# Performance work log

Hardware: AMD Instinct MI355X
Metric: run time of the kernel (lower is better)

Reference implementation:

```python
import jax, jax.numpy as jnp
import numpy as np

B, P, H, V, E, D = 32, 24, 24, 32000, 300, 512


def setup_inputs() -> dict:
    key = jax.random.key(0)
    ks = jax.random.split(key, 16)
    f32 = jnp.float32

    def nrm(k, shape, fan):
        return jax.random.normal(k, shape, f32) / np.sqrt(fan).astype(np.float32)

    return {
        'premise': jax.random.randint(ks[0], (B, P), 0, V),
        'hypothesis': jax.random.randint(ks[1], (B, H), 0, V),
        'embedding': jax.random.normal(ks[2], (V, E), f32),
        'W_ih': nrm(ks[3], (8 * D, 2 * E), 2 * E),
        'W_hh': nrm(ks[4], (8 * D, 2 * D), 2 * D),
        'b_ih': jnp.zeros((8 * D,), f32),
        'b_hh': jnp.zeros((8 * D,), f32),
        'W_ch': nrm(ks[5], (D, 2 * D), 2 * D),
        'b_ch': jnp.zeros((D,), f32),
        'W_cc': nrm(ks[6], (D, 2 * D), 2 * D),
        'b_cc': jnp.zeros((D,), f32),
        'W1': nrm(ks[7], (D, D), D),
        'b1': jnp.zeros((D,), f32),
        'W2': nrm(ks[8], (D, D), D),
        'b2': jnp.zeros((D,), f32),
        'W3': nrm(ks[9], (3, D), D),
        'b3': jnp.zeros((3,), f32),
    }


def reference(premise, hypothesis, embedding, W_ih, W_hh, b_ih, b_hh,
              W_ch, b_ch, W_cc, b_cc, W1, b1, W2, b2, W3, b3):
    prem = embedding[premise]      # [B,P,E]
    hyp = embedding[hypothesis]    # [B,H,E]
    bsz = prem.shape[0]
    d = W_ch.shape[0]
    prem_t = prem.transpose(1, 0, 2)  # [P,B,E]
    hyp_t = hyp.transpose(1, 0, 2)    # [H,B,E]
    zero = jnp.zeros((bsz, d), prem.dtype)

    def lstm_cell(x, h, c):
        # PyTorch LSTMCell gate order: i, f, g, o
        g = x @ W_ih.T + b_ih + h @ W_hh.T + b_hh
        i, f, gg, o = jnp.split(g, 4, axis=-1)
        c2 = jax.nn.sigmoid(f) * c + jax.nn.sigmoid(i) * jnp.tanh(gg)
        h2 = jax.nn.sigmoid(o) * jnp.tanh(c2)
        return h2, c2

    def outer(row, px):
        # row holds (h,c) of the previous premise row (left neighbors), [H,B,D]
        row_h, row_c = row

        def inner(low, ins):
            lh, lc = low                 # lower neighbor (current row, j-1)
            left_h, left_c, hx = ins     # left neighbor (prev row, j) and hyp emb
            x = jnp.concatenate([px, hx], axis=-1)          # [B,2E]
            hcat = jnp.concatenate([left_h, lh], axis=-1)   # [B,2D]
            ccat = jnp.concatenate([left_c, lc], axis=-1)
            oh, oc = lstm_cell(x, hcat, ccat)
            nh = oh @ W_ch.T + b_ch      # condense to [B,D]
            nc = oc @ W_cc.T + b_cc
            return (nh, nc), (nh, nc)

        _, (nrh, nrc) = jax.lax.scan(inner, (zero, zero), (row_h, row_c, hyp_t))
        return (nrh, nrc), None

    hlen = hyp_t.shape[0]
    init = (jnp.zeros((hlen, bsz, d), prem.dtype),
            jnp.zeros((hlen, bsz, d), prem.dtype))
    (row_h, _), _ = jax.lax.scan(outer, init, prem_t)

    h = row_h[-1]                          # h at grid cell (P,H)
    h = jax.nn.relu(h @ W1.T + b1)
    h = jax.nn.relu(h @ W2.T + b2)
    return jax.nn.softmax(h @ W3.T + b3, axis=1)
```

## Files before the change

kernel.cpp:

```cpp
#include <hip/hip_runtime.h>

#define P_   24
#define H_   24
#define E_   300
#define D_   512
#define TWOD 1024
#define G4   4096
#define SMEMB  27648
#define BUFSZ  23040
#define SMEMG2 46080

typedef __attribute__((ext_vector_type(8))) short bf16x8;
typedef __attribute__((ext_vector_type(4))) float f32x4;

__device__ __forceinline__ float bf2f(unsigned int u) {
    return __uint_as_float(u << 16);
}
__device__ __forceinline__ unsigned short f2bf(float f) {
    unsigned int x = __float_as_uint(f);
    unsigned int r = (x + 0x7fffu + ((x >> 16) & 1u)) >> 16;
    return (unsigned short)r;
}
__device__ __forceinline__ float sigf(float x) {
    return 1.0f / (1.0f + __expf(-x));
}
__device__ __forceinline__ float tanh_f(float x) {
    return 2.0f / (1.0f + __expf(-2.0f * x)) - 1.0f;
}

#define OFF_WHHP 0u
#define OFF_WCHB 8388608u
#define OFF_WCCB 9437184u
#define OFF_APRE 10485760u
#define OFF_CPRE 16777216u
#define OFF_PX   23068672u
#define OFF_HX   23560192u
#define OFF_HBB  24051712u
#define OFF_CBF  25624576u
#define OFF_H2B  28770304u
#define OFF_C2B  30343168u
#define OFF_HF   31916032u
#define OFF_T1   33488896u
#define OFF_T2   33554432u

__global__ __launch_bounds__(256) void k_p0(
        const int* __restrict__ prem, const int* __restrict__ hyp,
        const float* __restrict__ emb, const float* __restrict__ Whh,
        const float* __restrict__ Wch, const float* __restrict__ Wcc,
        char* __restrict__ wsb) {
    unsigned short* WhhP = (unsigned short*)(wsb + OFF_WHHP);
    unsigned short* WchB = (unsigned short*)(wsb + OFF_WCHB);
    unsigned short* WccB = (unsigned short*)(wsb + OFF_WCCB);
    unsigned short* PX   = (unsigned short*)(wsb + OFF_PX);
    unsigned short* HX   = (unsigned short*)(wsb + OFF_HX);

    int gt = blockIdx.x * 256 + threadIdx.x;
    int stride = gridDim.x * 256;
    for (int idx = gt; idx < 524288; idx += stride) {
        int n = idx >> 7;
        int k8 = (idx & 127) * 8;
        int q = n >> 10, rest = n & 1023;
        int nt = rest >> 5, u = rest & 31;
        int pr = nt * 128 + q * 32 + u;
        const float* s = Whh + (size_t)n * TWOD + k8;
        float4 va = *(const float4*)s, vb = *(const float4*)(s + 4);
        unsigned short o[8] = {f2bf(va.x), f2bf(va.y), f2bf(va.z), f2bf(va.w),
                               f2bf(vb.x), f2bf(vb.y), f2bf(vb.z), f2bf(vb.w)};
        *(uint4*)(WhhP + (size_t)pr * TWOD + k8) = *(const uint4*)o;
    }
    for (int idx = gt; idx < 131072; idx += stride) {
        int cc = idx & 65535;
        const float* s = ((idx < 65536) ? Wch : Wcc) + (size_t)cc * 8;
        unsigned short* dp = ((idx < 65536) ? WchB : WccB) + (size_t)cc * 8;
        float4 va = *(const float4*)s, vb = *(const float4*)(s + 4);
        unsigned short o[8] = {f2bf(va.x), f2bf(va.y), f2bf(va.z), f2bf(va.w),
                               f2bf(vb.x), f2bf(vb.y), f2bf(vb.z), f2bf(vb.w)};
        *(uint4*)dp = *(const uint4*)o;
    }
    for (int idx = gt; idx < 61440; idx += stride) {
        int isH = idx >= 30720 ? 1 : 0;
        int id2 = idx - isH * 30720;
        int rb = id2 / 40, c8 = (id2 % 40) * 8;
        int ri = rb >> 5, rbb = rb & 31;
        int tok = isH ? hyp[rbb * H_ + ri] : prem[rbb * P_ + ri];
        const float* s = emb + (size_t)tok * E_ + c8;
        unsigned short o[8];
        for (int e = 0; e < 8; ++e)
            o[e] = (c8 + e < E_) ? f2bf(s[e]) : (unsigned short)0;
        *(uint4*)((isH ? HX : PX) + rb * 320 + c8) = *(const uint4*)o;
    }
}

__global__ __launch_bounds__(256) void k_p1(
        const float* __restrict__ Wih, const float* __restrict__ bih,
        const float* __restrict__ bhh, char* __restrict__ wsb) {
    const unsigned short* PX = (const unsigned short*)(wsb + OFF_PX);
    const unsigned short* HX = (const unsigned short*)(wsb + OFF_HX);
    unsigned short* Apre = (unsigned short*)(wsb + OFF_APRE);
    unsigned short* Cpre = (unsigned short*)(wsb + OFF_CPRE);

    __shared__ __align__(16) unsigned char smem[SMEMB];
    const int t = threadIdx.x;
    const int lane = t & 63, wvi = t >> 6, l16 = lane & 15, quad = lane >> 4;
    const int wm = wvi >> 1, wn = wvi & 1;
    unsigned short (*At)[72] = (unsigned short (*)[72])smem;
    unsigned short (*Bt)[72] = (unsigned short (*)[72])(smem + 9216);

    int q = blockIdx.x;
    int x = q & 7, slot = q >> 3;
    int z = slot / 48, rem = slot % 48;
    int ntg = rem / 12, mt = rem % 12;
    int nt = ntg * 8 + x;
    const unsigned short* X = z ? HX : PX;
    int koff = z ? E_ : 0;
    unsigned short* Out = z ? Cpre : Apre;
    f32x4 acc[2][4] = {};
    int arow = t >> 2, acol = (t & 3) * 16;
    int brow = t >> 1, bcol = (t & 1) * 32;
    for (int s = 0; s < 5; ++s) {
        int k0 = s * 64;
        {
            const uint4* src = (const uint4*)(X + (size_t)(mt * 64 + arow) * 320 + k0 + acol);
            uint4* dst = (uint4*)&At[arow][acol];
            dst[0] = src[0]; dst[1] = src[1];
        }
        {
            int n = nt * 128 + brow;
            const float* wrow = Wih + (size_t)n * (2 * E_) + koff;
            unsigned short* dst = &Bt[brow][bcol];
            for (int c4 = 0; c4 < 8; ++c4) {
                int k = k0 + bcol + c4 * 4;
                if (k < E_) {
                    float4 v = *(const float4*)(wrow + k);
                    dst[c4 * 4 + 0] = f2bf(v.x); dst[c4 * 4 + 1] = f2bf(v.y);
                    dst[c4 * 4 + 2] = f2bf(v.z); dst[c4 * 4 + 3] = f2bf(v.w);
                } else {
                    dst[c4 * 4 + 0] = 0; dst[c4 * 4 + 1] = 0;
                    dst[c4 * 4 + 2] = 0; dst[c4 * 4 + 3] = 0;
                }
            }
        }
        __syncthreads();
        for (int ks = 0; ks < 2; ++ks) {
            bf16x8 a[2], bb[4];
            for (int mi = 0; mi < 2; ++mi)
                a[mi] = *(const bf16x8*)&At[wm * 32 + mi * 16 + l16][ks * 32 + quad * 8];
            for (int ni = 0; ni < 4; ++ni)
                bb[ni] = *(const bf16x8*)&Bt[wn * 64 + ni * 16 + l16][ks * 32 + quad * 8];
            for (int mi = 0; mi < 2; ++mi)
                for (int ni = 0; ni < 4; ++ni)
                    acc[mi][ni] = __builtin_amdgcn_mfma_f32_16x16x32_bf16(
                        a[mi], bb[ni], acc[mi][ni], 0, 0, 0);
        }
        __syncthreads();
    }
    for (int mi = 0; mi < 2; ++mi) {
        int rbase = mt * 64 + wm * 32 + mi * 16 + quad * 4;
        for (int ni = 0; ni < 4; ++ni) {
            int n = nt * 128 + wn * 64 + ni * 16 + l16;
            float bias = z ? 0.0f : (bih[n] + bhh[n]);
            for (int r = 0; r < 4; ++r)
                Out[(size_t)(rbase + r) * G4 + n] = f2bf(acc[mi][ni][r] + bias);
        }
    }
}

__global__ __launch_bounds__(256) void k_gates(int d, int ncells, char* __restrict__ wsb) {
    const unsigned short* WhhP = (const unsigned short*)(wsb + OFF_WHHP);
    const unsigned short* Apre = (const unsigned short*)(wsb + OFF_APRE);
    const unsigned short* Cpre = (const unsigned short*)(wsb + OFF_CPRE);
    const unsigned short* HbB  = (const unsigned short*)(wsb + OFF_HBB);
    const float*          Cbf  = (const float*)(wsb + OFF_CBF);
    unsigned short* H2B = (unsigned short*)(wsb + OFF_H2B);
    unsigned short* C2B = (unsigned short*)(wsb + OFF_C2B);

    int j_lo = (d > P_ - 1) ? d - (P_ - 1) : 0;

    int x = blockIdx.x & 7, slot = blockIdx.x >> 3;
    int ntg = slot / ncells, c = slot - ntg * ncells;
    int nt = ntg * 8 + x;
    int cj = j_lo + c, ci = d - cj;

    const unsigned short* HpB = HbB + (size_t)((d + 1) & 1) * (H_ * 32 * D_);
    const float* Cp = Cbf + (size_t)((d + 1) & 1) * (H_ * 32 * D_);

    __shared__ __align__(16) unsigned char smem[SMEMG2];
    const int t = threadIdx.x;
    const int lane = t & 63, wvi = t >> 6, l16 = lane & 15, quad = lane >> 4;

    f32x4 acc[2][2] = {};
    const int arow = t >> 3, acol = (t & 7) * 8;
    const int brow = t >> 1, bcol = (t & 1) * 32;
    const unsigned short* wsrc = WhhP + (size_t)(nt * 128 + brow) * TWOD + bcol;
    const unsigned short* asrcL =
        (ci > 0) ? HpB + (size_t)(cj * 32 + arow) * D_ : nullptr;
    const unsigned short* asrcD =
        (cj > 0) ? HpB + (size_t)((cj - 1) * 32 + arow) * D_ : nullptr;

    uint4 aR, bR0, bR1, bR2, bR3;
    #define LOAD_STEP(s_)                                                      \
        {                                                                      \
            int kk = (s_) * 64 + acol;                                         \
            const unsigned short* sp =                                         \
                (kk < D_) ? (asrcL ? asrcL + kk : nullptr)                     \
                          : (asrcD ? asrcD + (kk - D_) : nullptr);             \
            if (sp) aR = *(const uint4*)sp;                                    \
            else { aR.x = 0u; aR.y = 0u; aR.z = 0u; aR.w = 0u; }               \
            const uint4* s4 = (const uint4*)(wsrc + (s_) * 64);                \
            bR0 = s4[0]; bR1 = s4[1]; bR2 = s4[2]; bR3 = s4[3];                \
        }
    #define STORE_STEP(p_)                                                     \
        {                                                                      \
            unsigned short (*At_)[72] = (unsigned short (*)[72])(smem + (p_) * BUFSZ); \
            unsigned short (*Bt_)[72] = (unsigned short (*)[72])(smem + (p_) * BUFSZ + 4608); \
            *(uint4*)&At_[arow][acol] = aR;                                    \
            uint4* dp = (uint4*)&Bt_[brow][bcol];                              \
            dp[0] = bR0; dp[1] = bR1; dp[2] = bR2; dp[3] = bR3;                \
        }

    LOAD_STEP(0);
    STORE_STEP(0);
    __syncthreads();
    for (int s = 0; s < 16; ++s) {
        if (s < 15) LOAD_STEP(s + 1);
        int p = s & 1;
        unsigned short (*At)[72] = (unsigned short (*)[72])(smem + p * BUFSZ);
        unsigned short (*Bt)[72] = (unsigned short (*)[72])(smem + p * BUFSZ + 4608);
        for (int ks = 0; ks < 2; ++ks) {
            bf16x8 a0 = *(const bf16x8*)&At[l16][ks * 32 + quad * 8];
            bf16x8 a1 = *(const bf16x8*)&At[16 + l16][ks * 32 + quad * 8];
            bf16x8 b0 = *(const bf16x8*)&Bt[wvi * 32 + l16][ks * 32 + quad * 8];
            bf16x8 b1 = *(const bf16x8*)&Bt[wvi * 32 + 16 + l16][ks * 32 + quad * 8];
            acc[0][0] = __builtin_amdgcn_mfma_f32_16x16x32_bf16(a0, b0, acc[0][0], 0, 0, 0);
            acc[0][1] = __builtin_amdgcn_mfma_f32_16x16x32_bf16(a0, b1, acc[0][1], 0, 0, 0);
            acc[1][0] = __builtin_amdgcn_mfma_f32_16x16x32_bf16(a1, b0, acc[1][0], 0, 0, 0);
            acc[1][1] = __builtin_amdgcn_mfma_f32_16x16x32_bf16(a1, b1, acc[1][1], 0, 0, 0);
        }
        if (s < 15) {
            STORE_STEP(1 - p);
            __syncthreads();
        }
    }
    #undef LOAD_STEP
    #undef STORE_STEP

    float* Dt = (float*)smem;
    for (int mi = 0; mi < 2; ++mi)
        for (int ni = 0; ni < 2; ++ni) {
            int cc2 = wvi * 32 + ni * 16 + l16;
            int rr = mi * 16 + quad * 4;
            for (int r = 0; r < 4; ++r)
                Dt[(rr + r) * 132 + cc2] = acc[mi][ni][r];
        }
    __syncthreads();
    {
        int u = t & 31, r0 = (t >> 5) * 4;
        int k = nt * 32 + u;
        for (int r = r0; r < r0 + 4; ++r) {
            size_t ai = (size_t)(ci * 32 + r) * G4 + k;
            size_t cix = (size_t)(cj * 32 + r) * G4 + k;
            float g0 = Dt[r * 132 +      u] + bf2f(Apre[ai])        + bf2f(Cpre[cix]);
            float g1 = Dt[r * 132 + 32 + u] + bf2f(Apre[ai + 1024]) + bf2f(Cpre[cix + 1024]);
            float g2 = Dt[r * 132 + 64 + u] + bf2f(Apre[ai + 2048]) + bf2f(Cpre[cix + 2048]);
            float g3 = Dt[r * 132 + 96 + u] + bf2f(Apre[ai + 3072]) + bf2f(Cpre[cix + 3072]);
            float ccat;
            if (k < D_) ccat = (ci > 0) ? Cp[(size_t)(cj * 32 + r) * D_ + k] : 0.0f;
            else        ccat = (cj > 0) ? Cp[(size_t)((cj - 1) * 32 + r) * D_ + (k - D_)] : 0.0f;
            float si = sigf(g0), sf = sigf(g1), tg = tanh_f(g2), so = sigf(g3);
            float c2v = sf * ccat + si * tg;
            float h2v = so * tanh_f(c2v);
            H2B[(size_t)(c * 32 + r) * TWOD + k] = f2bf(h2v);
            C2B[(size_t)(c * 32 + r) * TWOD + k] = f2bf(c2v);
        }
    }
}

__global__ __launch_bounds__(256) void k_cond(
        int d, const float* __restrict__ bch, const float* __restrict__ bcc,
        char* __restrict__ wsb) {
    const unsigned short* H2B  = (const unsigned short*)(wsb + OFF_H2B);
    const unsigned short* C2B  = (const unsigned short*)(wsb + OFF_C2B);
    const unsigned short* WchB = (const unsigned short*)(wsb + OFF_WCHB);
    const unsigned short* WccB = (const unsigned short*)(wsb + OFF_WCCB);
    unsigned short* HbB = (unsigned short*)(wsb + OFF_HBB);
    float* Cbf = (float*)(wsb + OFF_CBF);
    float* Hf  = (float*)(wsb + OFF_HF);

    int j_lo = (d > P_ - 1) ? d - (P_ - 1) : 0;
    int xcd = blockIdx.x & 7, c = blockIdx.x >> 3;
    int z = xcd >> 2, ntile = xcd & 3;
    const unsigned short* Ain = z ? C2B : H2B;
    const unsigned short* W = z ? WccB : WchB;
    int cj = j_lo + c;

    __shared__ __align__(16) unsigned char smem[SMEMG2];
    const int t = threadIdx.x;
    const int lane = t & 63, wvi = t >> 6, l16 = lane & 15, quad = lane >> 4;

    unsigned short* HbC = HbB + (size_t)(d & 1) * (H_ * 32 * D_);
    float* CbC = Cbf + (size_t)(d & 1) * (H_ * 32 * D_);

    f32x4 acc[2][2] = {};
    const int arow = t >> 3, acol = (t & 7) * 8;
    const int brow = t >> 1, bcol = (t & 1) * 32;
    const unsigned short* asrc = Ain + (size_t)(c * 32 + arow) * TWOD + acol;
    const unsigned short* wsrc = W + (size_t)(ntile * 128 + brow) * TWOD + bcol;

    uint4 aR, bR0, bR1, bR2, bR3;
    #define LOAD_STEP(s_)                                                      \
        {                                                                      \
            aR = *(const uint4*)(asrc + (s_) * 64);                            \
            const uint4* s4 = (const uint4*)(wsrc + (s_) * 64);                \
            bR0 = s4[0]; bR1 = s4[1]; bR2 = s4[2]; bR3 = s4[3];                \
        }
    #define STORE_STEP(p_)                                                     \
        {                                                                      \
            unsigned short (*At_)[72] = (unsigned short (*)[72])(smem + (p_) * BUFSZ); \
            unsigned short (*Bt_)[72] = (unsigned short (*)[72])(smem + (p_) * BUFSZ + 4608); \
            *(uint4*)&At_[arow][acol] = aR;                                    \
            uint4* dp = (uint4*)&Bt_[brow][bcol];                              \
            dp[0] = bR0; dp[1] = bR1; dp[2] = bR2; dp[3] = bR3;                \
        }

    LOAD_STEP(0);
    STORE_STEP(0);
    __syncthreads();
    for (int s = 0; s < 16; ++s) {
        if (s < 15) LOAD_STEP(s + 1);
        int p = s & 1;
        unsigned short (*At)[72] = (unsigned short (*)[72])(smem + p * BUFSZ);
        unsigned short (*Bt)[72] = (unsigned short (*)[72])(smem + p * BUFSZ + 4608);
        for (int ks = 0; ks < 2; ++ks) {
            bf16x8 a0 = *(const bf16x8*)&At[l16][ks * 32 + quad * 8];
            bf16x8 a1 = *(const bf16x8*)&At[16 + l16][ks * 32 + quad * 8];
            bf16x8 b0 = *(const bf16x8*)&Bt[wvi * 32 + l16][ks * 32 + quad * 8];
            bf16x8 b1 = *(const bf16x8*)&Bt[wvi * 32 + 16 + l16][ks * 32 + quad * 8];
            acc[0][0] = __builtin_amdgcn_mfma_f32_16x16x32_bf16(a0, b0, acc[0][0], 0, 0, 0);
            acc[0][1] = __builtin_amdgcn_mfma_f32_16x16x32_bf16(a0, b1, acc[0][1], 0, 0, 0);
            acc[1][0] = __builtin_amdgcn_mfma_f32_16x16x32_bf16(a1, b0, acc[1][0], 0, 0, 0);
            acc[1][1] = __builtin_amdgcn_mfma_f32_16x16x32_bf16(a1, b1, acc[1][1], 0, 0, 0);
        }
        if (s < 15) {
            STORE_STEP(1 - p);
            __syncthreads();
        }
    }
    #undef LOAD_STEP
    #undef STORE_STEP

    for (int mi = 0; mi < 2; ++mi) {
        int rr = mi * 16 + quad * 4;
        for (int ni = 0; ni < 2; ++ni) {
            int n = ntile * 128 + wvi * 32 + ni * 16 + l16;
            float bsv = z ? bcc[n] : bch[n];
            for (int r = 0; r < 4; ++r) {
                int rb = rr + r;
                float val = acc[mi][ni][r] + bsv;
                if (z) {
                    CbC[(size_t)(cj * 32 + rb) * D_ + n] = val;
                } else {
                    HbC[(size_t)(cj * 32 + rb) * D_ + n] = f2bf(val);
                    if (d == P_ + H_ - 2)
                        Hf[(size_t)(cj * 32 + rb) * D_ + n] = val;
                }
            }
        }
    }
}

__global__ __launch_bounds__(256) void k_fc(
        const float* __restrict__ hin, const float* __restrict__ W,
        const float* __restrict__ bias, float* __restrict__ outv) {
    int g = blockIdx.x * 256 + threadIdx.x;
    int col = g & 511, rb = g >> 9;
    const float* h = hin + (size_t)rb * D_;
    const float* w = W + (size_t)col * D_;
    float accv = bias[col];
    for (int k = 0; k < D_; k += 4) {
        float4 wv4 = *(const float4*)(w + k);
        float4 hv = *(const float4*)(h + k);
        accv += hv.x * wv4.x + hv.y * wv4.y + hv.z * wv4.z + hv.w * wv4.w;
    }
    outv[(size_t)rb * D_ + col] = fmaxf(accv, 0.0f);
}

__global__ __launch_bounds__(128) void k_sm(
        const float* __restrict__ T2, const float* __restrict__ W3,
        const float* __restrict__ b3, float* __restrict__ out) {
    __shared__ float lg[96];
    int t = threadIdx.x;
    if (t < 96) {
        int rb = t / 3, cls = t % 3;
        const float* h = T2 + (size_t)rb * D_;
        const float* w = W3 + (size_t)cls * D_;
        float accv = b3[cls];
        for (int k = 0; k < D_; k += 4) {
            float4 wv4 = *(const float4*)(w + k);
            float4 hv = *(const float4*)(h + k);
            accv += hv.x * wv4.x + hv.y * wv4.y + hv.z * wv4.z + hv.w * wv4.w;
        }
        lg[rb * 3 + cls] = accv;
    }
    __syncthreads();
    if (t < 32) {
        float a = lg[t * 3 + 0], bq = lg[t * 3 + 1], cq = lg[t * 3 + 2];
        float m = fmaxf(a, fmaxf(bq, cq));
        float ea = __expf(a - m), eb = __expf(bq - m), ec = __expf(cq - m);
        float s = 1.0f / (ea + eb + ec);
        out[t * 3 + 0] = ea * s;
        out[t * 3 + 1] = eb * s;
        out[t * 3 + 2] = ec * s;
    }
}

extern "C" void kernel_launch(void* const* d_in, const int* in_sizes, int n_in,
                              void* d_out, int out_size, void* d_ws, size_t ws_size,
                              hipStream_t stream) {
    (void)in_sizes; (void)n_in; (void)out_size; (void)ws_size;

    const int* prem = (const int*)d_in[0];
    const int* hyp  = (const int*)d_in[1];
    const float* emb = (const float*)d_in[2];
    const float* Wih = (const float*)d_in[3];
    const float* Whh = (const float*)d_in[4];
    const float* bih = (const float*)d_in[5];
    const float* bhh = (const float*)d_in[6];
    const float* Wch = (const float*)d_in[7];
    const float* bch = (const float*)d_in[8];
    const float* Wcc = (const float*)d_in[9];
    const float* bcc = (const float*)d_in[10];
    const float* W1  = (const float*)d_in[11];
    const float* b1  = (const float*)d_in[12];
    const float* W2  = (const float*)d_in[13];
    const float* b2  = (const float*)d_in[14];
    const float* W3  = (const float*)d_in[15];
    const float* b3  = (const float*)d_in[16];
    float* outp = (float*)d_out;
    char* wsb = (char*)d_ws;

    float* Hf = (float*)(wsb + OFF_HF);
    float* T1 = (float*)(wsb + OFF_T1);
    float* T2 = (float*)(wsb + OFF_T2);

    k_p0<<<512, 256, 0, stream>>>(prem, hyp, emb, Whh, Wch, Wcc, wsb);
    k_p1<<<768, 256, 0, stream>>>(Wih, bih, bhh, wsb);
    for (int d = 0; d < P_ + H_ - 1; ++d) {
        int j_lo = (d > P_ - 1) ? d - (P_ - 1) : 0;
        int j_hi = (d < H_ - 1) ? d : H_ - 1;
        int ncells = j_hi - j_lo + 1;
        k_gates<<<ncells * 32, 256, 0, stream>>>(d, ncells, wsb);
        k_cond<<<ncells * 8, 256, 0, stream>>>(d, bch, bcc, wsb);
    }
    const float* hfin = Hf + (size_t)(H_ - 1) * 32 * D_;
    k_fc<<<64, 256, 0, stream>>>(hfin, W1, b1, T1);
    k_fc<<<64, 256, 0, stream>>>(T1, W2, b2, T2);
    k_sm<<<1, 128, 0, stream>>>(T2, W3, b3, outp);
}
```

Measured before the change: 1.609 ms.

## Replace per-diagonal kernel launches with a persistent cooperative kernel and grid barriers

The 94 per-diagonal gates/cond launches and the final FC and softmax launches are merged into one cooperative persistent kernel. Work is distributed as grid-strided jobs, and a hierarchical atomic grid barrier (per-XCD counters, then a global generation flag) separates the stages. This is meant to remove launch overhead and inter-kernel gaps on a long chain of small dependent steps. The risks are barrier latency, reduced occupancy from the fixed grid size, and dependence on cooperative launch support, with the old launch loop kept as a fallback.

```diff
diff --git a/kernel.cpp b/kernel.cpp
--- a/kernel.cpp
+++ b/kernel.cpp
@@ -42,6 +42,7 @@
 #define OFF_HF   31916032u
 #define OFF_T1   33488896u
 #define OFF_T2   33554432u
+#define OFF_BAR  33619968u
 
 __global__ __launch_bounds__(256) void k_p0(
         const int* __restrict__ prem, const int* __restrict__ hyp,
@@ -56,6 +57,7 @@
 
     int gt = blockIdx.x * 256 + threadIdx.x;
     int stride = gridDim.x * 256;
+    if (gt < 512) ((unsigned*)(wsb + OFF_BAR))[gt] = 0u;
     for (int idx = gt; idx < 524288; idx += stride) {
         int n = idx >> 7;
         int k8 = (idx & 127) * 8;
@@ -165,7 +167,9 @@
     }
 }
 
-__global__ __launch_bounds__(256) void k_gates(int d, int ncells, char* __restrict__ wsb) {
+__device__ __forceinline__ void gates_job(
+        int d, int ncells, int j_lo, int job,
+        char* __restrict__ wsb, unsigned char* smem) {
     const unsigned short* WhhP = (const unsigned short*)(wsb + OFF_WHHP);
     const unsigned short* Apre = (const unsigned short*)(wsb + OFF_APRE);
     const unsigned short* Cpre = (const unsigned short*)(wsb + OFF_CPRE);
@@ -174,9 +178,7 @@
     unsigned short* H2B = (unsigned short*)(wsb + OFF_H2B);
     unsigned short* C2B = (unsigned short*)(wsb + OFF_C2B);
 
-    int j_lo = (d > P_ - 1) ? d - (P_ - 1) : 0;
-
-    int x = blockIdx.x & 7, slot = blockIdx.x >> 3;
+    int x = job & 7, slot = job >> 3;
     int ntg = slot / ncells, c = slot - ntg * ncells;
     int nt = ntg * 8 + x;
     int cj = j_lo + c, ci = d - cj;
@@ -184,7 +186,6 @@
     const unsigned short* HpB = HbB + (size_t)((d + 1) & 1) * (H_ * 32 * D_);
     const float* Cp = Cbf + (size_t)((d + 1) & 1) * (H_ * 32 * D_);
 
-    __shared__ __align__(16) unsigned char smem[SMEMG2];
     const int t = threadIdx.x;
     const int lane = t & 63, wvi = t >> 6, l16 = lane & 15, quad = lane >> 4;
 
@@ -273,11 +274,13 @@
             C2B[(size_t)(c * 32 + r) * TWOD + k] = f2bf(c2v);
         }
     }
-}
-
-__global__ __launch_bounds__(256) void k_cond(
-        int d, const float* __restrict__ bch, const float* __restrict__ bcc,
-        char* __restrict__ wsb) {
+    __syncthreads();
+}
+
+__device__ __forceinline__ void cond_job(
+        int d, int j_lo, int job,
+        const float* __restrict__ bch, const float* __restrict__ bcc,
+        char* __restrict__ wsb, unsigned char* smem) {
     const unsigned short* H2B  = (const unsigned short*)(wsb + OFF_H2B);
     const unsigned short* C2B  = (const unsigned short*)(wsb + OFF_C2B);
     const unsigned short* WchB = (const unsigned short*)(wsb + OFF_WCHB);
@@ -286,14 +289,12 @@
     float* Cbf = (float*)(wsb + OFF_CBF);
     float* Hf  = (float*)(wsb + OFF_HF);
 
-    int j_lo = (d > P_ - 1) ? d - (P_ - 1) : 0;
-    int xcd = blockIdx.x & 7, c = blockIdx.x >> 3;
+    int xcd = job & 7, c = job >> 3;
     int z = xcd >> 2, ntile = xcd & 3;
     const unsigned short* Ain = z ? C2B : H2B;
     const unsigned short* W = z ? WccB : WchB;
     int cj = j_lo + c;
 
-    __shared__ __align__(16) unsigned char smem[SMEMG2];
     const int t = threadIdx.x;
     const int lane = t & 63, wvi = t >> 6, l16 = lane & 15, quad = lane >> 4;
 
@@ -368,10 +369,10 @@
     }
 }
 
-__global__ __launch_bounds__(256) void k_fc(
+__device__ __forceinline__ void fc_job(
         const float* __restrict__ hin, const float* __restrict__ W,
-        const float* __restrict__ bias, float* __restrict__ outv) {
-    int g = blockIdx.x * 256 + threadIdx.x;
+        const float* __restrict__ bias, float* __restrict__ outv, int job) {
+    int g = job * 256 + threadIdx.x;
     int col = g & 511, rb = g >> 9;
     const float* h = hin + (size_t)rb * D_;
     const float* w = W + (size_t)col * D_;
@@ -384,10 +385,9 @@
     outv[(size_t)rb * D_ + col] = fmaxf(accv, 0.0f);
 }
 
-__global__ __launch_bounds__(128) void k_sm(
+__device__ __forceinline__ void sm_job(
         const float* __restrict__ T2, const float* __restrict__ W3,
-        const float* __restrict__ b3, float* __restrict__ out) {
-    __shared__ float lg[96];
+        const float* __restrict__ b3, float* __restrict__ out, float* lg) {
     int t = threadIdx.x;
     if (t < 96) {
         int rb = t / 3, cls = t % 3;
@@ -411,6 +411,92 @@
         out[t * 3 + 1] = eb * s;
         out[t * 3 + 2] = ec * s;
     }
+}
+
+__device__ __forceinline__ void grid_barrier(unsigned* bs, unsigned gen) {
+    __syncthreads();
+    if (threadIdx.x == 0) {
+        const unsigned gs = gridDim.x >> 3;
+        unsigned* gcnt = bs + ((blockIdx.x & 7u) << 5);
+        unsigned old = __hip_atomic_fetch_add(gcnt, 1u, __ATOMIC_ACQ_REL,
+                                              __HIP_MEMORY_SCOPE_AGENT);
+        if (old == gs - 1u) {
+            __hip_atomic_store(gcnt, 0u, __ATOMIC_RELAXED,
+                               __HIP_MEMORY_SCOPE_AGENT);
+            unsigned oc = __hip_atomic_fetch_add(bs + 288, 1u, __ATOMIC_ACQ_REL,
+                                                 __HIP_MEMORY_SCOPE_AGENT);
+            if (oc == 7u) {
+                __hip_atomic_store(bs + 288, 0u, __ATOMIC_RELAXED,
+                                   __HIP_MEMORY_SCOPE_AGENT);
+                __hip_atomic_store(bs + 320, gen + 1u, __ATOMIC_RELEASE,
+                                   __HIP_MEMORY_SCOPE_AGENT);
+            }
+        }
+        while (__hip_atomic_load(bs + 320, __ATOMIC_RELAXED,
+                                 __HIP_MEMORY_SCOPE_AGENT) == gen)
+            __builtin_amdgcn_s_sleep(4);
+        (void)__hip_atomic_load(bs + 320, __ATOMIC_ACQUIRE,
+                                __HIP_MEMORY_SCOPE_AGENT);
+    }
+    __syncthreads();
+}
+
+__global__ __launch_bounds__(256) void k_loop(
+        const float* __restrict__ bch, const float* __restrict__ bcc,
+        const float* __restrict__ W1, const float* __restrict__ b1,
+        const float* __restrict__ W2, const float* __restrict__ b2,
+        const float* __restrict__ W3, const float* __restrict__ b3,
+        float* __restrict__ outp, char* __restrict__ wsb) {
+    __shared__ __align__(16) unsigned char smem[SMEMG2];
+    unsigned* bs = (unsigned*)(wsb + OFF_BAR);
+    const int grid = gridDim.x;
+    unsigned bgen = 0;
+    for (int d = 0; d < P_ + H_ - 1; ++d) {
+        int j_lo = (d > P_ - 1) ? d - (P_ - 1) : 0;
+        int j_hi = (d < H_ - 1) ? d : H_ - 1;
+        int ncells = j_hi - j_lo + 1;
+        for (int job = blockIdx.x; job < ncells * 32; job += grid)
+            gates_job(d, ncells, j_lo, job, wsb, smem);
+        grid_barrier(bs, bgen); ++bgen;
+        for (int job = blockIdx.x; job < ncells * 8; job += grid)
+            cond_job(d, j_lo, job, bch, bcc, wsb, smem);
+        grid_barrier(bs, bgen); ++bgen;
+    }
+    const float* hfin = (const float*)(wsb + OFF_HF) + (size_t)(H_ - 1) * 32 * D_;
+    float* T1 = (float*)(wsb + OFF_T1);
+    float* T2 = (float*)(wsb + OFF_T2);
+    if (blockIdx.x < 64) fc_job(hfin, W1, b1, T1, blockIdx.x);
+    grid_barrier(bs, bgen); ++bgen;
+    if (blockIdx.x < 64) fc_job(T1, W2, b2, T2, blockIdx.x);
+    grid_barrier(bs, bgen); ++bgen;
+    if (blockIdx.x == 0) sm_job(T2, W3, b3, outp, (float*)smem);
+}
+
+__global__ __launch_bounds__(256) void k_gates(int d, int ncells, char* __restrict__ wsb) {
+    __shared__ __align__(16) unsigned char smem[SMEMG2];
+    int j_lo = (d > P_ - 1) ? d - (P_ - 1) : 0;
+    gates_job(d, ncells, j_lo, blockIdx.x, wsb, smem);
+}
+
+__global__ __launch_bounds__(256) void k_cond(
+        int d, const float* __restrict__ bch, const float* __restrict__ bcc,
+        char* __restrict__ wsb) {
+    __shared__ __align__(16) unsigned char smem[SMEMG2];
+    int j_lo = (d > P_ - 1) ? d - (P_ - 1) : 0;
+    cond_job(d, j_lo, blockIdx.x, bch, bcc, wsb, smem);
+}
+
+__global__ __launch_bounds__(256) void k_fc(
+        const float* __restrict__ hin, const float* __restrict__ W,
+        const float* __restrict__ bias, float* __restrict__ outv) {
+    fc_job(hin, W, bias, outv, blockIdx.x);
+}
+
+__global__ __launch_bounds__(128) void k_sm(
+        const float* __restrict__ T2, const float* __restrict__ W3,
+        const float* __restrict__ b3, float* __restrict__ out) {
+    __shared__ float lg[96];
+    sm_job(T2, W3, b3, out, lg);
 }
 
 extern "C" void kernel_launch(void* const* d_in, const int* in_sizes, int n_in,
@@ -438,21 +524,37 @@
     float* outp = (float*)d_out;
     char* wsb = (char*)d_ws;
 
-    float* Hf = (float*)(wsb + OFF_HF);
-    float* T1 = (float*)(wsb + OFF_T1);
-    float* T2 = (float*)(wsb + OFF_T2);
-
     k_p0<<<512, 256, 0, stream>>>(prem, hyp, emb, Whh, Wch, Wcc, wsb);
     k_p1<<<768, 256, 0, stream>>>(Wih, bih, bhh, wsb);
-    for (int d = 0; d < P_ + H_ - 1; ++d) {
-        int j_lo = (d > P_ - 1) ? d - (P_ - 1) : 0;
-        int j_hi = (d < H_ - 1) ? d : H_ - 1;
-        int ncells = j_hi - j_lo + 1;
-        k_gates<<<ncells * 32, 256, 0, stream>>>(d, ncells, wsb);
-        k_cond<<<ncells * 8, 256, 0, stream>>>(d, bch, bcc, wsb);
-    }
-    const float* hfin = Hf + (size_t)(H_ - 1) * 32 * D_;
-    k_fc<<<64, 256, 0, stream>>>(hfin, W1, b1, T1);
-    k_fc<<<64, 256, 0, stream>>>(T1, W2, b2, T2);
-    k_sm<<<1, 128, 0, stream>>>(T2, W3, b3, outp);
-}
+
+    bool ok = false;
+    {
+        int maxb = 0;
+        if (hipOccupancyMaxActiveBlocksPerMultiprocessor(
+                &maxb, reinterpret_cast<const void*>(k_loop), 256, 0) == hipSuccess &&
+            maxb > 0) {
+            int grid = (maxb >= 3) ? 768 : (maxb == 2 ? 512 : 256);
+            void* args[] = {(void*)&bch, (void*)&bcc, (void*)&W1, (void*)&b1,
+                            (void*)&W2,  (void*)&b2,  (void*)&W3, (void*)&b3,
+                            (void*)&outp, (void*)&wsb};
+            ok = hipLaunchCooperativeKernel(reinterpret_cast<const void*>(k_loop),
+                                            dim3(grid), dim3(256), args, 0,
+                                            stream) == hipSuccess;
+        }
+    }
+    if (!ok) {
+        for (int d = 0; d < P_ + H_ - 1; ++d) {
+            int j_lo = (d > P_ - 1) ? d - (P_ - 1) : 0;
+            int j_hi = (d < H_ - 1) ? d : H_ - 1;
+            int ncells = j_hi - j_lo + 1;
+            k_gates<<<ncells * 32, 256, 0, stream>>>(d, ncells, wsb);
+            k_cond<<<ncells * 8, 256, 0, stream>>>(d, bch, bcc, wsb);
+        }
+        float* T1 = (float*)(wsb + OFF_T1);
+        float* T2 = (float*)(wsb + OFF_T2);
+        const float* hfin = (const float*)(wsb + OFF_HF) + (size_t)(H_ - 1) * 32 * D_;
+        k_fc<<<64, 256, 0, stream>>>(hfin, W1, b1, T1);
+        k_fc<<<64, 256, 0, stream>>>(T1, W2, b2, T2);
+        k_sm<<<1, 128, 0, stream>>>(T2, W3, b3, outp);
+    }
+}
```

After: 3.148 ms. 95.7% more time.
